# Performance work log

Measured on AMD Instinct MI355X. Metric: run time of the kernel, lower is better.

The kernel has to match this reference:

```python
import jax, jax.numpy as jnp
import numpy as np

B, N, F_IN, F_OUT = 8, 2048, 64, 64
NEG_SLOPE = 0.01  # torch F.leaky_relu default


def setup_inputs() -> dict:
    key = jax.random.key(0)
    k_h, k_W, k_a = jax.random.split(key, 3)
    h = jax.random.normal(k_h, (B, N, F_IN), dtype=jnp.float32)
    adj = jnp.ones((B, N, N), dtype=jnp.float32)  # unused by the math, kept for signature fidelity
    # xavier_uniform init
    lim_W = float(np.sqrt(6.0 / (F_IN + F_OUT)))
    W = jax.random.uniform(k_W, (F_IN, F_OUT), minval=-lim_W, maxval=lim_W, dtype=jnp.float32)
    lim_a = float(np.sqrt(6.0 / (2 * F_OUT + 1)))
    a = jax.random.uniform(k_a, (2 * F_OUT, 1), minval=-lim_a, maxval=lim_a, dtype=jnp.float32)
    return {"h": h, "adj": adj, "W": W, "a": a}


def reference(h, adj, W, a):
    # Wh: [B, N, F_out]
    Wh = jnp.matmul(h, W)
    f_out = W.shape[1]
    # Exact decomposition of a^T [Wh_i || Wh_j] = a1.Wh_i + a2.Wh_j
    a1 = a[:f_out, 0]
    a2 = a[f_out:, 0]
    f1 = Wh @ a1  # [B, N] scores for source node i
    f2 = Wh @ a2  # [B, N] scores for target node j
    e = jax.nn.leaky_relu(f1[:, :, None] + f2[:, None, :], NEG_SLOPE)  # [B, N, N]
    attention = jax.nn.softmax(e, axis=-1)  # softmax over j (adj is NOT used, as in the source)
    h_prime = jnp.einsum('bij,bjf->bif', attention, Wh)
    return h_prime
```

## Files before the change

### kernel.cpp

```cpp
#include <hip/hip_runtime.h>
#include <math.h>

#define BB 8
#define NN 2048
#define FF 64

__global__ __launch_bounds__(256) void k1_gemm(const float* __restrict__ h,
                                               const float* __restrict__ W,
                                               const float* __restrict__ a,
                                               float* __restrict__ Wh,
                                               float* __restrict__ f1,
                                               float* __restrict__ f2) {
  __shared__ float Wl[FF * FF];
  __shared__ float hl[4 * FF];
  __shared__ float a1l[FF], a2l[FF];
  const int tid = threadIdx.x;
  const int r = tid >> 6, f = tid & 63;
  for (int i = tid; i < FF * FF; i += 256) Wl[i] = W[i];
  if (tid < FF) { a1l[tid] = a[tid]; a2l[tid] = a[FF + tid]; }
  const int row0 = blockIdx.x * 4;
  for (int i = tid; i < 4 * FF; i += 256) hl[i] = h[(size_t)row0 * FF + i];
  __syncthreads();
  const int row = row0 + r;
  float acc = 0.f;
#pragma unroll
  for (int k = 0; k < FF; ++k) acc = fmaf(hl[r * FF + k], Wl[k * FF + f], acc);
  Wh[(size_t)row * FF + f] = acc;
  float v1 = acc * a1l[f];
  float v2 = acc * a2l[f];
#pragma unroll
  for (int o = 32; o > 0; o >>= 1) {
    v1 += __shfl_xor(v1, o, 64);
    v2 += __shfl_xor(v2, o, 64);
  }
  if (f == 0) { f1[row] = v1; f2[row] = v2; }
}

__global__ __launch_bounds__(1024) void k2_sort(const float* __restrict__ f2,
                                                float* __restrict__ f2s,
                                                int* __restrict__ idxs) {
  __shared__ float key[NN];
  __shared__ int val[NN];
  const int b = blockIdx.x, tid = threadIdx.x;
  for (int i = tid; i < NN; i += 1024) { key[i] = f2[b * NN + i]; val[i] = i; }
  __syncthreads();
  for (int k = 2; k <= NN; k <<= 1) {
    for (int j = k >> 1; j > 0; j >>= 1) {
      for (int i = tid; i < NN; i += 1024) {
        const int ixj = i ^ j;
        if (ixj > i) {
          const bool up = ((i & k) == 0);
          const float ki = key[i], kj = key[ixj];
          if ((ki > kj) == up) {
            key[i] = kj; key[ixj] = ki;
            const int vi = val[i]; val[i] = val[ixj]; val[ixj] = vi;
          }
        }
      }
      __syncthreads();
    }
  }
  for (int i = tid; i < NN; i += 1024) {
    f2s[b * NN + i] = key[i];
    idxs[b * NN + i] = val[i];
  }
}

__global__ __launch_bounds__(256) void k3_scan(const float* __restrict__ Wh,
                                               const float* __restrict__ f2s,
                                               const int* __restrict__ idxs,
                                               float* __restrict__ S_hi,
                                               float* __restrict__ P_lo,
                                               float* __restrict__ Sz,
                                               float* __restrict__ Pz) {
  __shared__ double sl[256];
  const int fi = blockIdx.x;
  const int b = blockIdx.y;
  const int t = threadIdx.x;
  const float* f2b = f2s + (size_t)b * NN;
  const int* idb = idxs + (size_t)b * NN;

  {
    double v[8]; double s = 0.0;
#pragma unroll
    for (int i = 0; i < 8; ++i) {
      const int q = t * 8 + i;
      const double w = exp(0.01 * (double)f2b[q]);
      const double vv = (fi < FF) ? (double)Wh[((size_t)b * NN + idb[q]) * FF + fi] : 1.0;
      v[i] = w * vv; s += v[i];
    }
    sl[t] = s; __syncthreads();
    for (int off = 1; off < 256; off <<= 1) {
      const double add = (t >= off) ? sl[t - off] : 0.0;
      __syncthreads();
      sl[t] += add;
      __syncthreads();
    }
    double run = (t > 0) ? sl[t - 1] : 0.0;
    const double tot = sl[255];
#pragma unroll
    for (int i = 0; i < 8; ++i) {
      const int q = t * 8 + i;
      if (fi < FF) P_lo[((size_t)b * (NN + 1) + q) * FF + fi] = (float)run;
      else         Pz[(size_t)b * (NN + 1) + q] = (float)run;
      run += v[i];
    }
    if (t == 255) {
      if (fi < FF) P_lo[((size_t)b * (NN + 1) + NN) * FF + fi] = (float)tot;
      else         Pz[(size_t)b * (NN + 1) + NN] = (float)tot;
    }
    __syncthreads();
  }

  {
    double v[8]; double s = 0.0;
#pragma unroll
    for (int i = 0; i < 8; ++i) {
      const int q = NN - 1 - (t * 8 + i);
      const double w = exp((double)f2b[q]);
      const double vv = (fi < FF) ? (double)Wh[((size_t)b * NN + idb[q]) * FF + fi] : 1.0;
      v[i] = w * vv; s += v[i];
    }
    sl[t] = s; __syncthreads();
    for (int off = 1; off < 256; off <<= 1) {
      const double add = (t >= off) ? sl[t - off] : 0.0;
      __syncthreads();
      sl[t] += add;
      __syncthreads();
    }
    double run = (t > 0) ? sl[t - 1] : 0.0;
#pragma unroll
    for (int i = 0; i < 8; ++i) {
      const int q = NN - 1 - (t * 8 + i);
      const double inc = run + v[i];
      if (fi < FF) S_hi[((size_t)b * (NN + 1) + q) * FF + fi] = (float)inc;
      else         Sz[(size_t)b * (NN + 1) + q] = (float)inc;
      run = inc;
    }
    if (t == 0) {
      if (fi < FF) S_hi[((size_t)b * (NN + 1) + NN) * FF + fi] = 0.f;
      else         Sz[(size_t)b * (NN + 1) + NN] = 0.f;
    }
  }
}

__global__ __launch_bounds__(256) void k4_out(const float* __restrict__ f1,
                                              const float* __restrict__ f2s,
                                              const float* __restrict__ S_hi,
                                              const float* __restrict__ P_lo,
                                              const float* __restrict__ Sz,
                                              const float* __restrict__ Pz,
                                              float* __restrict__ out) {
  const int tid = threadIdx.x;
  const int r = tid >> 6, f = tid & 63;
  const int row = blockIdx.x * 4 + r;
  const int b = row >> 11;
  const float* f2b = f2s + (size_t)b * NN;
  const float f1v = f1[row];
  const float t = -f1v;
  int lo = 0, hi = NN;
  while (lo < hi) {
    const int mid = (lo + hi) >> 1;
    if (f2b[mid] < t) lo = mid + 1; else hi = mid;
  }
  const int p0 = lo;
  const double w1 = exp((double)f1v);
  const double w2 = exp(0.01 * (double)f1v);
  const size_t bp = (size_t)b * (NN + 1) + p0;
  const double num = w1 * (double)S_hi[bp * FF + f] + w2 * (double)P_lo[bp * FF + f];
  const double Z = w1 * (double)Sz[bp] + w2 * (double)Pz[bp];
  out[(size_t)row * FF + f] = (float)(num / Z);
}

extern "C" void kernel_launch(void* const* d_in, const int* in_sizes, int n_in,
                              void* d_out, int out_size, void* d_ws, size_t ws_size,
                              hipStream_t stream) {
  const float* h = (const float*)d_in[0];
  const float* W = (const float*)d_in[2];
  const float* a = (const float*)d_in[3];
  float* out = (float*)d_out;

  float* ws = (float*)d_ws;
  size_t o = 0;
  float* Wh  = ws + o; o += (size_t)BB * NN * FF;
  float* f1  = ws + o; o += (size_t)BB * NN;
  float* f2  = ws + o; o += (size_t)BB * NN;
  float* f2s = ws + o; o += (size_t)BB * NN;
  int*   idxs = (int*)(ws + o); o += (size_t)BB * NN;
  float* S_hi = ws + o; o += (size_t)BB * (NN + 1) * FF;
  float* P_lo = ws + o; o += (size_t)BB * (NN + 1) * FF;
  float* Sz  = ws + o; o += (size_t)BB * (NN + 1);
  float* Pz  = ws + o; o += (size_t)BB * (NN + 1);

  k1_gemm<<<BB * NN / 4, 256, 0, stream>>>(h, W, a, Wh, f1, f2);
  k2_sort<<<BB, 1024, 0, stream>>>(f2, f2s, idxs);
  dim3 g3(FF + 1, BB);
  k3_scan<<<g3, 256, 0, stream>>>(Wh, f2s, idxs, S_hi, P_lo, Sz, Pz);
  k4_out<<<BB * NN / 4, 256, 0, stream>>>(f1, f2s, S_hi, P_lo, Sz, Pz, out);
}
```

Baseline: 258.2 us.

## Restructure prefix scans as coalesced chunked scans and precompute weights and search positions

The scan kernel changes from one block per feature column, doing strided gathers and a log-step shared-memory scan, to two 1024-thread blocks per batch. Each wave handles a 128-element chunk across all 64 features with coalesced row reads, then combines chunk totals in shared memory. The sort kernel now also computes the double-precision exp weights and the per-row binary-search split point, so the scan and output kernels no longer repeat that work. The trade-off is parallelism: only 16 scan blocks run, each doing long serial loops, and the sort kernel's 8 blocks take on extra work.

```diff
diff --git a/kernel.cpp b/kernel.cpp
--- a/kernel.cpp
+++ b/kernel.cpp
@@ -37,8 +37,11 @@
 }
 
 __global__ __launch_bounds__(1024) void k2_sort(const float* __restrict__ f2,
-                                                float* __restrict__ f2s,
-                                                int* __restrict__ idxs) {
+                                                const float* __restrict__ f1,
+                                                int* __restrict__ idxs,
+                                                double* __restrict__ wlo,
+                                                double* __restrict__ whi,
+                                                int* __restrict__ p0arr) {
   __shared__ float key[NN];
   __shared__ int val[NN];
   const int b = blockIdx.x, tid = threadIdx.x;
@@ -61,91 +64,94 @@
     }
   }
   for (int i = tid; i < NN; i += 1024) {
-    f2s[b * NN + i] = key[i];
     idxs[b * NN + i] = val[i];
-  }
-}
-
-__global__ __launch_bounds__(256) void k3_scan(const float* __restrict__ Wh,
-                                               const float* __restrict__ f2s,
-                                               const int* __restrict__ idxs,
-                                               float* __restrict__ S_hi,
-                                               float* __restrict__ P_lo,
-                                               float* __restrict__ Sz,
-                                               float* __restrict__ Pz) {
-  __shared__ double sl[256];
-  const int fi = blockIdx.x;
+    const double k = (double)key[i];
+    wlo[b * NN + i] = exp(0.01 * k);
+    whi[b * NN + i] = exp(k);
+  }
+  for (int i = tid; i < NN; i += 1024) {
+    const float t = -f1[b * NN + i];
+    int lo = 0, hi = NN;
+    while (lo < hi) { const int m = (lo + hi) >> 1; if (key[m] < t) lo = m + 1; else hi = m; }
+    p0arr[b * NN + i] = lo;
+  }
+}
+
+__global__ __launch_bounds__(1024) void k3_scan(const float* __restrict__ Wh,
+                                                const int* __restrict__ idxs,
+                                                const double* __restrict__ wlo,
+                                                const double* __restrict__ whi,
+                                                float* __restrict__ P_lo,
+                                                float* __restrict__ S_hi,
+                                                float* __restrict__ Pz,
+                                                float* __restrict__ Sz) {
+  __shared__ double sl[16][64];
+  __shared__ double slz[16];
+  const int pass = blockIdx.x;
   const int b = blockIdx.y;
-  const int t = threadIdx.x;
-  const float* f2b = f2s + (size_t)b * NN;
-  const int* idb = idxs + (size_t)b * NN;
-
-  {
-    double v[8]; double s = 0.0;
-#pragma unroll
-    for (int i = 0; i < 8; ++i) {
-      const int q = t * 8 + i;
-      const double w = exp(0.01 * (double)f2b[q]);
-      const double vv = (fi < FF) ? (double)Wh[((size_t)b * NN + idb[q]) * FF + fi] : 1.0;
-      v[i] = w * vv; s += v[i];
-    }
-    sl[t] = s; __syncthreads();
-    for (int off = 1; off < 256; off <<= 1) {
-      const double add = (t >= off) ? sl[t - off] : 0.0;
-      __syncthreads();
-      sl[t] += add;
-      __syncthreads();
-    }
-    double run = (t > 0) ? sl[t - 1] : 0.0;
-    const double tot = sl[255];
-#pragma unroll
-    for (int i = 0; i < 8; ++i) {
-      const int q = t * 8 + i;
-      if (fi < FF) P_lo[((size_t)b * (NN + 1) + q) * FF + fi] = (float)run;
-      else         Pz[(size_t)b * (NN + 1) + q] = (float)run;
-      run += v[i];
-    }
-    if (t == 255) {
-      if (fi < FF) P_lo[((size_t)b * (NN + 1) + NN) * FF + fi] = (float)tot;
-      else         Pz[(size_t)b * (NN + 1) + NN] = (float)tot;
-    }
+  const int tid = threadIdx.x;
+  const int f = tid & 63, c = tid >> 6;
+  const int q0 = c * 128;
+  const int* __restrict__ idb = idxs + b * NN;
+  const float* __restrict__ Whb = Wh + (size_t)b * NN * FF;
+
+  if (pass == 0) {
+    const double* __restrict__ wv = wlo + b * NN;
+    double s = 0.0, sz = 0.0;
+#pragma unroll 4
+    for (int i = 0; i < 128; ++i) {
+      const int q = q0 + i;
+      const double w = wv[q];
+      s += w * (double)Whb[(size_t)idb[q] * FF + f];
+      sz += w;
+    }
+    sl[c][f] = s; if (f == 0) slz[c] = sz;
     __syncthreads();
-  }
-
-  {
-    double v[8]; double s = 0.0;
-#pragma unroll
-    for (int i = 0; i < 8; ++i) {
-      const int q = NN - 1 - (t * 8 + i);
-      const double w = exp((double)f2b[q]);
-      const double vv = (fi < FF) ? (double)Wh[((size_t)b * NN + idb[q]) * FF + fi] : 1.0;
-      v[i] = w * vv; s += v[i];
-    }
-    sl[t] = s; __syncthreads();
-    for (int off = 1; off < 256; off <<= 1) {
-      const double add = (t >= off) ? sl[t - off] : 0.0;
-      __syncthreads();
-      sl[t] += add;
-      __syncthreads();
-    }
-    double run = (t > 0) ? sl[t - 1] : 0.0;
-#pragma unroll
-    for (int i = 0; i < 8; ++i) {
-      const int q = NN - 1 - (t * 8 + i);
-      const double inc = run + v[i];
-      if (fi < FF) S_hi[((size_t)b * (NN + 1) + q) * FF + fi] = (float)inc;
-      else         Sz[(size_t)b * (NN + 1) + q] = (float)inc;
-      run = inc;
-    }
-    if (t == 0) {
-      if (fi < FF) S_hi[((size_t)b * (NN + 1) + NN) * FF + fi] = 0.f;
-      else         Sz[(size_t)b * (NN + 1) + NN] = 0.f;
-    }
+    double run = 0.0, runz = 0.0;
+    for (int cc = 0; cc < c; ++cc) { run += sl[cc][f]; runz += slz[cc]; }
+    float* __restrict__ P = P_lo + (size_t)b * (NN + 1) * FF;
+    float* __restrict__ PzB = Pz + (size_t)b * (NN + 1);
+#pragma unroll 4
+    for (int i = 0; i < 128; ++i) {
+      const int q = q0 + i;
+      P[(size_t)q * FF + f] = (float)run;
+      if (f == 0) PzB[q] = (float)runz;
+      const double w = wv[q];
+      run += w * (double)Whb[(size_t)idb[q] * FF + f];
+      runz += w;
+    }
+    if (c == 15) { P[(size_t)NN * FF + f] = (float)run; if (f == 0) PzB[NN] = (float)runz; }
+  } else {
+    const double* __restrict__ wv = whi + b * NN;
+    double s = 0.0, sz = 0.0;
+#pragma unroll 4
+    for (int i = 0; i < 128; ++i) {
+      const int q = q0 + i;
+      const double w = wv[q];
+      s += w * (double)Whb[(size_t)idb[q] * FF + f];
+      sz += w;
+    }
+    sl[c][f] = s; if (f == 0) slz[c] = sz;
+    __syncthreads();
+    double run = 0.0, runz = 0.0;
+    for (int cc = c + 1; cc < 16; ++cc) { run += sl[cc][f]; runz += slz[cc]; }
+    float* __restrict__ S = S_hi + (size_t)b * (NN + 1) * FF;
+    float* __restrict__ SzB = Sz + (size_t)b * (NN + 1);
+#pragma unroll 4
+    for (int i = 127; i >= 0; --i) {
+      const int q = q0 + i;
+      const double w = wv[q];
+      run += w * (double)Whb[(size_t)idb[q] * FF + f];
+      runz += w;
+      S[(size_t)q * FF + f] = (float)run;
+      if (f == 0) SzB[q] = (float)runz;
+    }
+    if (c == 15) { S[(size_t)NN * FF + f] = 0.f; if (f == 0) SzB[NN] = 0.f; }
   }
 }
 
 __global__ __launch_bounds__(256) void k4_out(const float* __restrict__ f1,
-                                              const float* __restrict__ f2s,
+                                              const int* __restrict__ p0arr,
                                               const float* __restrict__ S_hi,
                                               const float* __restrict__ P_lo,
                                               const float* __restrict__ Sz,
@@ -155,15 +161,8 @@
   const int r = tid >> 6, f = tid & 63;
   const int row = blockIdx.x * 4 + r;
   const int b = row >> 11;
-  const float* f2b = f2s + (size_t)b * NN;
   const float f1v = f1[row];
-  const float t = -f1v;
-  int lo = 0, hi = NN;
-  while (lo < hi) {
-    const int mid = (lo + hi) >> 1;
-    if (f2b[mid] < t) lo = mid + 1; else hi = mid;
-  }
-  const int p0 = lo;
+  const int p0 = p0arr[row];
   const double w1 = exp((double)f1v);
   const double w2 = exp(0.01 * (double)f1v);
   const size_t bp = (size_t)b * (NN + 1) + p0;
@@ -185,16 +184,18 @@
   float* Wh  = ws + o; o += (size_t)BB * NN * FF;
   float* f1  = ws + o; o += (size_t)BB * NN;
   float* f2  = ws + o; o += (size_t)BB * NN;
-  float* f2s = ws + o; o += (size_t)BB * NN;
   int*   idxs = (int*)(ws + o); o += (size_t)BB * NN;
+  double* wlo = (double*)(ws + o); o += (size_t)BB * NN * 2;
+  double* whi = (double*)(ws + o); o += (size_t)BB * NN * 2;
+  int*   p0arr = (int*)(ws + o); o += (size_t)BB * NN;
   float* S_hi = ws + o; o += (size_t)BB * (NN + 1) * FF;
   float* P_lo = ws + o; o += (size_t)BB * (NN + 1) * FF;
   float* Sz  = ws + o; o += (size_t)BB * (NN + 1);
   float* Pz  = ws + o; o += (size_t)BB * (NN + 1);
 
   k1_gemm<<<BB * NN / 4, 256, 0, stream>>>(h, W, a, Wh, f1, f2);
-  k2_sort<<<BB, 1024, 0, stream>>>(f2, f2s, idxs);
-  dim3 g3(FF + 1, BB);
-  k3_scan<<<g3, 256, 0, stream>>>(Wh, f2s, idxs, S_hi, P_lo, Sz, Pz);
-  k4_out<<<BB * NN / 4, 256, 0, stream>>>(f1, f2s, S_hi, P_lo, Sz, Pz, out);
-}
+  k2_sort<<<BB, 1024, 0, stream>>>(f2, f1, idxs, wlo, whi, p0arr);
+  dim3 g3(2, BB);
+  k3_scan<<<g3, 1024, 0, stream>>>(Wh, idxs, wlo, whi, P_lo, S_hi, Pz, Sz);
+  k4_out<<<BB * NN / 4, 256, 0, stream>>>(f1, p0arr, S_hi, P_lo, Sz, Pz, out);
+}
```

Result: slower. 283.1 us (+9.7%).
